# Kernel tuning notes

Hardware: AMD Instinct MI355X
Metric: run time of the kernel (lower is better)

Reference implementation:

```python
import jax, jax.numpy as jnp
import numpy as np

N, F, H, E, C1, C2, NCLS, K = 10000, 64, 128, 640000, 100, 1, 2, 3


def _spmm(rows, cols, vals, x, n):
    # sparse [n,n] @ dense [n,F] via edge list: out[r] += v * x[c]
    return jax.ops.segment_sum(vals[:, None] * x[cols], rows, num_segments=n)


def _cluster(xc, W1, b1, W2, b2):
    # ClusteringLayer: soft assignment s [m,c]; pooled feats [c,F]; corr at input res [m,F]
    h = jax.nn.relu(xc @ W1 + b1)
    s = jax.nn.softmax(h @ W2 + b2, axis=1)
    x_new = s.T @ xc
    corr = s @ x_new
    return x_new, corr, s


def setup_inputs() -> dict:
    key = jax.random.key(0)
    ks = jax.random.split(key, 20)
    sc = 0.05
    return {
        "x": jax.random.normal(ks[0], (N, F), jnp.float32),
        "x_cov": jax.random.normal(ks[1], (N, F), jnp.float32),
        "edge_index": jax.random.randint(ks[2], (2, E), 0, N),
        "adj_vals": jax.random.uniform(ks[3], (E,), jnp.float32),
        "norm_vals": jax.random.uniform(ks[4], (E,), jnp.float32) / 64.0,
        "feature_corr": jax.random.normal(ks[5], (1, F), jnp.float32),
        "bn_gamma": jnp.ones((F,), jnp.float32),
        "bn_beta": jnp.zeros((F,), jnp.float32),
        "pool0_W1": sc * jax.random.normal(ks[6], (F, H), jnp.float32),
        "pool0_b1": jnp.zeros((H,), jnp.float32),
        "pool0_W2": sc * jax.random.normal(ks[7], (H, C1), jnp.float32),
        "pool0_b2": jnp.zeros((C1,), jnp.float32),
        "pool1_W1": sc * jax.random.normal(ks[8], (F, H), jnp.float32),
        "pool1_b1": jnp.zeros((H,), jnp.float32),
        "pool1_W2": sc * jax.random.normal(ks[9], (H, C2), jnp.float32),
        "pool1_b2": jnp.zeros((C2,), jnp.float32),
        "mlp_W1": sc * jax.random.normal(ks[10], (F, H), jnp.float32),
        "mlp_b1": jnp.zeros((H,), jnp.float32),
        "mlp_W2": sc * jax.random.normal(ks[11], (H, H), jnp.float32),
        "mlp_b2": jnp.zeros((H,), jnp.float32),
        "mlp_W3": sc * jax.random.normal(ks[12], (H, NCLS), jnp.float32),
        "mlp_b3": jnp.zeros((NCLS,), jnp.float32),
        "prelu_a": jnp.asarray(0.25, jnp.float32),
    }


def reference(x, x_cov, edge_index, adj_vals, norm_vals, feature_corr,
              bn_gamma, bn_beta,
              pool0_W1, pool0_b1, pool0_W2, pool0_b2,
              pool1_W1, pool1_b1, pool1_W2, pool1_b2,
              mlp_W1, mlp_b1, mlp_W2, mlp_b2, mlp_W3, mlp_b3, prelu_a):
    rows, cols = edge_index[0], edge_index[1]
    n = x.shape[0]
    # BatchNorm1d (batch statistics)
    mu = x.mean(axis=0)
    var = x.var(axis=0)
    x = x0 = (x - mu) / jnp.sqrt(var + 1e-5) * bn_gamma + bn_beta
    # hierarchical pooling (n_pool = 2)
    x_cov1, corr0, s0 = _cluster(x_cov, pool0_W1, pool0_b1, pool0_W2, pool0_b2)   # s0 [N,C1]
    x_cov2, corr1, s1 = _cluster(x_cov1, pool1_W1, pool1_b1, pool1_W2, pool1_b2)  # s1 [C1,1]
    # gains (i=1): 2*sigmoid(masks[1] @ corrs[2] - corrs[1])  -> [C1,F]
    g0 = 2.0 * jax.nn.sigmoid(s1 @ feature_corr - corr1)
    # per-edge diag-mask values: m[e,f] = sum_c s0[r_e,c] * g0[c,f] * s0[c_e,c]
    m = (s0[rows] * s0[cols]) @ g0                      # [E,F]
    # adj is cumulatively multiplied across the feature loop j (adj reused across j)
    adjs = adj_vals[:, None] * jnp.cumprod(m, axis=1)   # [E,F] sparse values on adj pattern
    # Propagation with alpha=0: x = norm_adj @ x, k times (x0 contributes alpha*x0 = 0)
    for _ in range(K):
        x = _spmm(rows, cols, norm_vals, x, n)
    prelu = lambda z: jnp.where(z > 0, z, prelu_a * z)
    h = prelu(x @ mlp_W1 + mlp_b1)
    h = prelu(h @ mlp_W2 + mlp_b2)
    logits = h @ mlp_W3 + mlp_b3
    return jax.nn.log_softmax(logits, axis=1), adjs
```

## Files before the change

### kernel.cpp

```cpp
#include <hip/hip_runtime.h>

#define NN 10000
#define FF 64
#define HH 128
#define EE 640000
#define CC 100

__global__ __launch_bounds__(256) void k_bn_stats(
    const float* __restrict__ x, const float* __restrict__ gamma,
    const float* __restrict__ beta, float* __restrict__ scale, float* __restrict__ shift){
  int f = blockIdx.x, t = threadIdx.x;
  double s = 0.0, s2 = 0.0;
  for (int r = t; r < NN; r += 256){ float v = x[r*FF + f]; s += v; s2 += (double)v * v; }
  #pragma unroll
  for (int o = 32; o > 0; o >>= 1){ s += __shfl_down(s, o); s2 += __shfl_down(s2, o); }
  __shared__ double ls[4], ls2[4];
  if ((t & 63) == 0){ ls[t >> 6] = s; ls2[t >> 6] = s2; }
  __syncthreads();
  if (t == 0){
    double S  = ls[0]+ls[1]+ls[2]+ls[3];
    double S2 = ls2[0]+ls2[1]+ls2[2]+ls2[3];
    double mu = S / NN;
    double var = S2 / NN - mu*mu;
    double sc = (double)gamma[f] / sqrt(var + 1e-5);
    scale[f] = (float)sc;
    shift[f] = (float)((double)beta[f] - mu*sc);
  }
}

__global__ __launch_bounds__(256) void k_hist(const int* __restrict__ rows, int* __restrict__ counts){
  int e = blockIdx.x*256 + threadIdx.x;
  if (e < EE) atomicAdd(&counts[rows[e]], 1);
}

__global__ __launch_bounds__(256) void k_scan(const int* __restrict__ counts,
    int* __restrict__ offs, int* __restrict__ curs){
  __shared__ int part[256];
  int t = threadIdx.x;
  int base = t*40;
  int s = 0;
  for (int i=0;i<40;i++){ int idx=base+i; if (idx<NN) s += counts[idx]; }
  part[t] = s;
  __syncthreads();
  for (int o=1;o<256;o<<=1){
    int v = (t>=o)? part[t-o] : 0;
    __syncthreads();
    part[t] += v;
    __syncthreads();
  }
  int run = (t==0)? 0 : part[t-1];
  for (int i=0;i<40;i++){ int idx=base+i; if (idx<NN){ offs[idx]=run; curs[idx]=run; run += counts[idx]; } }
  if (t==255) offs[NN] = part[255];
}

__global__ __launch_bounds__(256) void k_scatter(const int* __restrict__ rows, const int* __restrict__ cols,
    const float* __restrict__ nvals, int* __restrict__ curs,
    int* __restrict__ cols_s, float* __restrict__ vals_s){
  int e = blockIdx.x*256 + threadIdx.x;
  if (e < EE){
    int r = rows[e];
    int pos = atomicAdd(&curs[r], 1);
    cols_s[pos] = cols[e];
    vals_s[pos] = nvals[e];
  }
}

__global__ __launch_bounds__(256) void k_spmm_bn(
    const int* __restrict__ offs, const int* __restrict__ cols_s, const float* __restrict__ vals_s,
    const float* __restrict__ xin, const float* __restrict__ scale, const float* __restrict__ shift,
    float* __restrict__ xout){
  int lane = threadIdx.x & 63;
  int r = blockIdx.x*4 + (threadIdx.x >> 6);
  float sc = scale[lane], sh = shift[lane];
  int b = offs[r], e = offs[r+1];
  float acc = 0.f;
  for (int j = b; j < e; ++j){
    int c = cols_s[j]; float v = vals_s[j];
    acc += v * (xin[c*FF + lane]*sc + sh);
  }
  xout[r*FF + lane] = acc;
}

__global__ __launch_bounds__(256) void k_spmm(
    const int* __restrict__ offs, const int* __restrict__ cols_s, const float* __restrict__ vals_s,
    const float* __restrict__ xin, float* __restrict__ xout){
  int lane = threadIdx.x & 63;
  int r = blockIdx.x*4 + (threadIdx.x >> 6);
  int b = offs[r], e = offs[r+1];
  float acc = 0.f;
  for (int j = b; j < e; ++j){
    int c = cols_s[j];
    acc += vals_s[j] * xin[c*FF + lane];
  }
  xout[r*FF + lane] = acc;
}

__global__ __launch_bounds__(256) void k_s0(
    const float* __restrict__ xcov,
    const float* __restrict__ W1, const float* __restrict__ b1,
    const float* __restrict__ W2, const float* __restrict__ b2,
    float* __restrict__ s0){
  __shared__ float xs[32][FF];
  __shared__ float hs[32][HH];
  __shared__ float lsm[32][CC];
  __shared__ float chunk[32*HH];
  __shared__ float rsum[32];
  int t = threadIdx.x; int r0 = blockIdx.x*32;
  for (int i=t;i<32*FF;i+=256){ int r=i>>6, f=i&63; int gr=r0+r; xs[r][f] = (gr<NN)? xcov[gr*FF+f] : 0.f; }
  __syncthreads();
  {
    int j = t & 127;
    float acc[16]; float bb = b1[j];
    #pragma unroll
    for (int p=0;p<16;p++) acc[p] = bb;
    for (int kc=0;kc<2;kc++){
      for (int i=t;i<32*HH;i+=256) chunk[i] = W1[(kc*32 + (i>>7))*HH + (i&127)];
      __syncthreads();
      #pragma unroll
      for (int p=0;p<16;p++){
        int r = (t>>7) + 2*p;
        float a = acc[p];
        #pragma unroll
        for (int k=0;k<32;k++) a += xs[r][kc*32+k]*chunk[k*HH + j];
        acc[p] = a;
      }
      __syncthreads();
    }
    #pragma unroll
    for (int p=0;p<16;p++){ int r=(t>>7)+2*p; hs[r][j] = fmaxf(acc[p], 0.f); }
  }
  __syncthreads();
  {
    float acc[13];
    #pragma unroll
    for (int p=0;p<13;p++){ int i=p*256+t; acc[p] = (i<3200)? b2[i % CC] : 0.f; }
    for (int kc=0;kc<4;kc++){
      for (int i=t;i<32*CC;i+=256) chunk[i] = W2[(kc*32 + i/CC)*CC + (i % CC)];
      __syncthreads();
      #pragma unroll
      for (int p=0;p<13;p++){
        int i = p*256+t;
        if (i < 32*CC){
          int r = i/CC, j = i - r*CC;
          float a = acc[p];
          #pragma unroll
          for (int k=0;k<32;k++) a += hs[r][kc*32+k]*chunk[k*CC + j];
          acc[p] = a;
        }
      }
      __syncthreads();
    }
    #pragma unroll
    for (int p=0;p<13;p++){ int i=p*256+t; if (i<32*CC){ int r=i/CC, j=i-r*CC; lsm[r][j]=acc[p]; } }
  }
  __syncthreads();
  if (t < 32){
    float m = -1e30f;
    for (int j=0;j<CC;j++) m = fmaxf(m, lsm[t][j]);
    float s = 0.f;
    for (int j=0;j<CC;j++){ float e = expf(lsm[t][j]-m); lsm[t][j]=e; s += e; }
    rsum[t] = s;
  }
  __syncthreads();
  for (int i=t;i<32*CC;i+=256){ int r=i/CC, j=i-r*CC; int gr=r0+r; if (gr<NN) s0[gr*CC + j] = lsm[r][j]/rsum[r]; }
}

__global__ __launch_bounds__(256) void k_xcov1(
    const float* __restrict__ s0, const float* __restrict__ xcov, float* __restrict__ xc1){
  __shared__ float srow[4][CC];
  __shared__ float xrow[4][FF];
  int t = threadIdx.x;
  int rbase = blockIdx.x * 100;
  int f = t & 63, cb = (t>>6)*25;
  float acc[25];
  #pragma unroll
  for (int i=0;i<25;i++) acc[i]=0.f;
  for (int step=0; step<25; ++step){
    int rr0 = rbase + step*4;
    for (int i=t;i<4*CC;i+=256){ int rr=i/CC; srow[rr][i - rr*CC] = s0[(rr0+rr)*CC + (i - rr*CC)]; }
    for (int i=t;i<4*FF;i+=256){ int rr=i>>6; xrow[rr][i&63] = xcov[(rr0+rr)*FF + (i&63)]; }
    __syncthreads();
    #pragma unroll
    for (int rr=0;rr<4;rr++){
      float xv = xrow[rr][f];
      #pragma unroll
      for (int i=0;i<25;i++) acc[i] += srow[rr][cb+i]*xv;
    }
    __syncthreads();
  }
  #pragma unroll
  for (int i=0;i<25;i++) atomicAdd(&xc1[(cb+i)*FF + f], acc[i]);
}

__global__ void k_gv(const float* __restrict__ xc1, const float* __restrict__ fc, float* __restrict__ gv){
  int f = threadIdx.x;
  float s = 0.f;
  for (int c=0;c<CC;c++) s += xc1[c*FF + f];
  float z = fc[f] - s;
  gv[f] = 2.f / (1.f + expf(-z));
}

__global__ __launch_bounds__(256) void k_adjs(
    const int* __restrict__ rows, const int* __restrict__ cols,
    const float* __restrict__ adjv, const float* __restrict__ s0,
    const float* __restrict__ gv, float* __restrict__ out){
  __shared__ float gvs[64];
  __shared__ int   rs[256], cs[256];
  __shared__ float dotbuf[256];
  __shared__ float buf[16*258];
  int t = threadIdx.x;
  int e0 = blockIdx.x*256;
  rs[t] = rows[e0+t]; cs[t] = cols[e0+t];
  if (t < 64) gvs[t] = gv[t];
  __syncthreads();
  int gid = t>>4, lane = t&15;
  for (int it=0; it<16; ++it){
    int ed = gid*16 + it;
    int r = rs[ed], c = cs[ed];
    const float2* sr = (const float2*)(s0 + (size_t)r*CC);
    const float2* sc2 = (const float2*)(s0 + (size_t)c*CC);
    float p = 0.f;
    #pragma unroll
    for (int k=0;k<4;k++){
      int cc2 = k*16 + lane;
      if (cc2 < 50){
        float2 a = sr[cc2], b = sc2[cc2];
        p += a.x*b.x + a.y*b.y;
      }
    }
    #pragma unroll
    for (int o=1;o<16;o<<=1) p += __shfl_xor(p, o);
    if (lane==0) dotbuf[ed] = p;
  }
  __syncthreads();
  float dot = dotbuf[t];
  float adj = adjv[e0+t];
  float cum = 1.f;
  float4* out4 = (float4*)out;
  size_t obase4 = (size_t)e0*16;
  for (int ch=0; ch<4; ++ch){
    #pragma unroll
    for (int j=0;j<16;j++){
      cum *= dot * gvs[ch*16+j];
      buf[j*258 + t] = adj*cum;
    }
    __syncthreads();
    #pragma unroll
    for (int i=0;i<4;i++){
      int id = i*256 + t;
      int el = id >> 2, f4 = id & 3;
      float4 v;
      v.x = buf[(f4*4+0)*258 + el];
      v.y = buf[(f4*4+1)*258 + el];
      v.z = buf[(f4*4+2)*258 + el];
      v.w = buf[(f4*4+3)*258 + el];
      out4[obase4 + (size_t)el*16 + ch*4 + f4] = v;
    }
    __syncthreads();
  }
}

__global__ __launch_bounds__(256) void k_mlp(
    const float* __restrict__ xin,
    const float* __restrict__ W1, const float* __restrict__ b1,
    const float* __restrict__ W2, const float* __restrict__ b2,
    const float* __restrict__ W3, const float* __restrict__ b3,
    const float* __restrict__ pa, float* __restrict__ out){
  __shared__ float xs[32][FF];
  __shared__ float h1[32][HH];
  __shared__ float h2[32][HH];
  __shared__ float chunk[32*HH];
  __shared__ float lg[32][2];
  int t = threadIdx.x; int r0 = blockIdx.x*32;
  float a0 = pa[0];
  for (int i=t;i<32*FF;i+=256){ int r=i>>6,f=i&63; int gr=r0+r; xs[r][f]=(gr<NN)? xin[gr*FF+f] : 0.f; }
  __syncthreads();
  {
    int j = t & 127;
    float acc[16]; float bb=b1[j];
    #pragma unroll
    for (int p=0;p<16;p++) acc[p]=bb;
    for (int kc=0;kc<2;kc++){
      for (int i=t;i<32*HH;i+=256) chunk[i]=W1[(kc*32+(i>>7))*HH+(i&127)];
      __syncthreads();
      #pragma unroll
      for (int p=0;p<16;p++){ int r=(t>>7)+2*p; float a=acc[p];
        #pragma unroll
        for (int k=0;k<32;k++) a += xs[r][kc*32+k]*chunk[k*HH+j];
        acc[p]=a; }
      __syncthreads();
    }
    #pragma unroll
    for (int p=0;p<16;p++){ int r=(t>>7)+2*p; float v=acc[p]; h1[r][j] = v>0.f? v : a0*v; }
  }
  __syncthreads();
  {
    int j = t & 127;
    float acc[16]; float bb=b2[j];
    #pragma unroll
    for (int p=0;p<16;p++) acc[p]=bb;
    for (int kc=0;kc<4;kc++){
      for (int i=t;i<32*HH;i+=256) chunk[i]=W2[(kc*32+(i>>7))*HH+(i&127)];
      __syncthreads();
      #pragma unroll
      for (int p=0;p<16;p++){ int r=(t>>7)+2*p; float a=acc[p];
        #pragma unroll
        for (int k=0;k<32;k++) a += h1[r][kc*32+k]*chunk[k*HH+j];
        acc[p]=a; }
      __syncthreads();
    }
    #pragma unroll
    for (int p=0;p<16;p++){ int r=(t>>7)+2*p; float v=acc[p]; h2[r][j] = v>0.f? v : a0*v; }
  }
  __syncthreads();
  if (t < 64){
    int cls = t & 1, r = t >> 1;
    float acc = b3[cls];
    #pragma unroll
    for (int k=0;k<HH;k++){
      int kk = (k + r) & 127;
      acc += h2[r][kk]*W3[kk*2+cls];
    }
    lg[r][cls] = acc;
  }
  __syncthreads();
  if (t < 32){
    int gr = r0 + t;
    if (gr < NN){
      float l0=lg[t][0], l1=lg[t][1];
      float m = fmaxf(l0,l1);
      float lse = m + logf(expf(l0-m)+expf(l1-m));
      out[gr*2+0] = l0 - lse;
      out[gr*2+1] = l1 - lse;
    }
  }
}

extern "C" void kernel_launch(void* const* d_in, const int* in_sizes, int n_in,
                              void* d_out, int out_size, void* d_ws, size_t ws_size,
                              hipStream_t stream) {
  (void)in_sizes; (void)n_in; (void)out_size; (void)ws_size;
  const float* x      = (const float*)d_in[0];
  const float* xcov   = (const float*)d_in[1];
  const int*   ei     = (const int*)d_in[2];
  const float* adjv   = (const float*)d_in[3];
  const float* nvals  = (const float*)d_in[4];
  const float* fc     = (const float*)d_in[5];
  const float* gamma  = (const float*)d_in[6];
  const float* beta   = (const float*)d_in[7];
  const float* p0W1   = (const float*)d_in[8];
  const float* p0b1   = (const float*)d_in[9];
  const float* p0W2   = (const float*)d_in[10];
  const float* p0b2   = (const float*)d_in[11];
  const float* mW1    = (const float*)d_in[16];
  const float* mb1    = (const float*)d_in[17];
  const float* mW2    = (const float*)d_in[18];
  const float* mb2    = (const float*)d_in[19];
  const float* mW3    = (const float*)d_in[20];
  const float* mb3    = (const float*)d_in[21];
  const float* pa     = (const float*)d_in[22];
  const int* rows = ei;
  const int* cols = ei + EE;
  float* out = (float*)d_out;

  char* w = (char*)d_ws;
  auto alloc = [&](size_t bytes)->void*{ void* p=(void*)w; w += (bytes + 255) & ~(size_t)255; return p; };
  float* S0    = (float*)alloc(sizeof(float)*(size_t)NN*CC);
  float* XC1   = (float*)alloc(sizeof(float)*CC*FF);
  float* GV    = (float*)alloc(sizeof(float)*FF);
  float* SCALE = (float*)alloc(sizeof(float)*FF);
  float* SHIFT = (float*)alloc(sizeof(float)*FF);
  float* XA    = (float*)alloc(sizeof(float)*(size_t)NN*FF);
  float* XB    = (float*)alloc(sizeof(float)*(size_t)NN*FF);
  int*   COUNTS= (int*)alloc(sizeof(int)*NN);
  int*   OFFS  = (int*)alloc(sizeof(int)*(NN+1));
  int*   CURS  = (int*)alloc(sizeof(int)*NN);
  int*   COLS_S= (int*)alloc(sizeof(int)*EE);
  float* VALS_S= (float*)alloc(sizeof(float)*EE);

  hipMemsetAsync(COUNTS, 0, sizeof(int)*NN, stream);
  hipMemsetAsync(XC1, 0, sizeof(float)*CC*FF, stream);

  k_bn_stats<<<FF, 256, 0, stream>>>(x, gamma, beta, SCALE, SHIFT);
  k_hist<<<EE/256, 256, 0, stream>>>(rows, COUNTS);
  k_scan<<<1, 256, 0, stream>>>(COUNTS, OFFS, CURS);
  k_scatter<<<EE/256, 256, 0, stream>>>(rows, cols, nvals, CURS, COLS_S, VALS_S);

  k_s0<<<(NN+31)/32, 256, 0, stream>>>(xcov, p0W1, p0b1, p0W2, p0b2, S0);
  k_xcov1<<<100, 256, 0, stream>>>(S0, xcov, XC1);
  k_gv<<<1, 64, 0, stream>>>(XC1, fc, GV);
  k_adjs<<<EE/256, 256, 0, stream>>>(rows, cols, adjv, S0, GV, out + 2*NN);

  k_spmm_bn<<<NN/4, 256, 0, stream>>>(OFFS, COLS_S, VALS_S, x, SCALE, SHIFT, XA);
  k_spmm   <<<NN/4, 256, 0, stream>>>(OFFS, COLS_S, VALS_S, XA, XB);
  k_spmm   <<<NN/4, 256, 0, stream>>>(OFFS, COLS_S, VALS_S, XB, XA);

  k_mlp<<<(NN+31)/32, 256, 0, stream>>>(XA, mW1, mb1, mW2, mb2, mW3, mb3, pa, out);
}
```

Measured before the change: 690.3 us.

## Parallelize BN stats, split adjs into dot and stream kernels, unroll SpMM

Batch-norm statistics become a 100-block partial reduction followed by a small finishing kernel, replacing the 64-block per-feature column walk. The scan widens to 1024 threads. The SpMM loops unroll by four with independent accumulators to expose more memory-level parallelism. The per-edge s0 dot products move to their own kernel that uses float4 loads and writes to a new buffer, which the adjs kernel then streams. The s0 and MLP kernels are also reworked: weights are cached in registers, loads are vectorized, and the softmax and logits use shuffle reductions. The extra dot buffer adds an EE-sized write and read, and the new launches add overhead.

```diff
diff --git a/kernel.cpp b/kernel.cpp
--- a/kernel.cpp
+++ b/kernel.cpp
@@ -6,26 +6,35 @@
 #define EE 640000
 #define CC 100
 
-__global__ __launch_bounds__(256) void k_bn_stats(
-    const float* __restrict__ x, const float* __restrict__ gamma,
-    const float* __restrict__ beta, float* __restrict__ scale, float* __restrict__ shift){
-  int f = blockIdx.x, t = threadIdx.x;
+__global__ __launch_bounds__(256) void k_bn_partial(
+    const float* __restrict__ x, double* __restrict__ part){
+  __shared__ double ds[4][64], d2[4][64];
+  int t = threadIdx.x; int f = t & 63, g = t >> 6;
+  size_t base = (size_t)blockIdx.x * 6400;
   double s = 0.0, s2 = 0.0;
-  for (int r = t; r < NN; r += 256){ float v = x[r*FF + f]; s += v; s2 += (double)v * v; }
   #pragma unroll
-  for (int o = 32; o > 0; o >>= 1){ s += __shfl_down(s, o); s2 += __shfl_down(s2, o); }
-  __shared__ double ls[4], ls2[4];
-  if ((t & 63) == 0){ ls[t >> 6] = s; ls2[t >> 6] = s2; }
-  __syncthreads();
-  if (t == 0){
-    double S  = ls[0]+ls[1]+ls[2]+ls[3];
-    double S2 = ls2[0]+ls2[1]+ls2[2]+ls2[3];
-    double mu = S / NN;
-    double var = S2 / NN - mu*mu;
-    double sc = (double)gamma[f] / sqrt(var + 1e-5);
-    scale[f] = (float)sc;
-    shift[f] = (float)((double)beta[f] - mu*sc);
-  }
+  for (int i = 0; i < 25; i++){ float v = x[base + i*256 + t]; s += v; s2 += (double)v * v; }
+  ds[g][f] = s; d2[g][f] = s2;
+  __syncthreads();
+  if (t < 64){
+    double S  = ds[0][t]+ds[1][t]+ds[2][t]+ds[3][t];
+    double S2 = d2[0][t]+d2[1][t]+d2[2][t]+d2[3][t];
+    part[blockIdx.x*128 + t]      = S;
+    part[blockIdx.x*128 + 64 + t] = S2;
+  }
+}
+
+__global__ void k_bn_finish(const double* __restrict__ part,
+    const float* __restrict__ gamma, const float* __restrict__ beta,
+    float* __restrict__ scale, float* __restrict__ shift){
+  int f = threadIdx.x;
+  double S = 0.0, S2 = 0.0;
+  for (int b = 0; b < 100; b++){ S += part[b*128 + f]; S2 += part[b*128 + 64 + f]; }
+  double mu = S / NN;
+  double var = S2 / NN - mu*mu;
+  double sc = (double)gamma[f] / sqrt(var + 1e-5);
+  scale[f] = (float)sc;
+  shift[f] = (float)((double)beta[f] - mu*sc);
 }
 
 __global__ __launch_bounds__(256) void k_hist(const int* __restrict__ rows, int* __restrict__ counts){
@@ -33,24 +42,26 @@
   if (e < EE) atomicAdd(&counts[rows[e]], 1);
 }
 
-__global__ __launch_bounds__(256) void k_scan(const int* __restrict__ counts,
+__global__ __launch_bounds__(1024) void k_scan(const int* __restrict__ counts,
     int* __restrict__ offs, int* __restrict__ curs){
-  __shared__ int part[256];
+  __shared__ int part[1024];
   int t = threadIdx.x;
-  int base = t*40;
+  int base = t*10;
   int s = 0;
-  for (int i=0;i<40;i++){ int idx=base+i; if (idx<NN) s += counts[idx]; }
+  #pragma unroll
+  for (int i=0;i<10;i++){ int idx=base+i; if (idx<NN) s += counts[idx]; }
   part[t] = s;
   __syncthreads();
-  for (int o=1;o<256;o<<=1){
+  for (int o=1;o<1024;o<<=1){
     int v = (t>=o)? part[t-o] : 0;
     __syncthreads();
     part[t] += v;
     __syncthreads();
   }
   int run = (t==0)? 0 : part[t-1];
-  for (int i=0;i<40;i++){ int idx=base+i; if (idx<NN){ offs[idx]=run; curs[idx]=run; run += counts[idx]; } }
-  if (t==255) offs[NN] = part[255];
+  #pragma unroll
+  for (int i=0;i<10;i++){ int idx=base+i; if (idx<NN){ offs[idx]=run; curs[idx]=run; run += counts[idx]; } }
+  if (t==1023) offs[NN] = part[1023];
 }
 
 __global__ __launch_bounds__(256) void k_scatter(const int* __restrict__ rows, const int* __restrict__ cols,
@@ -73,12 +84,18 @@
   int r = blockIdx.x*4 + (threadIdx.x >> 6);
   float sc = scale[lane], sh = shift[lane];
   int b = offs[r], e = offs[r+1];
-  float acc = 0.f;
-  for (int j = b; j < e; ++j){
-    int c = cols_s[j]; float v = vals_s[j];
-    acc += v * (xin[c*FF + lane]*sc + sh);
-  }
-  xout[r*FF + lane] = acc;
+  float a0=0.f,a1=0.f,a2=0.f,a3=0.f;
+  int j = b;
+  for (; j+4<=e; j+=4){
+    int c0=cols_s[j],c1=cols_s[j+1],c2=cols_s[j+2],c3=cols_s[j+3];
+    float v0=vals_s[j],v1=vals_s[j+1],v2=vals_s[j+2],v3=vals_s[j+3];
+    a0 += v0*(xin[(size_t)c0*FF+lane]*sc+sh);
+    a1 += v1*(xin[(size_t)c1*FF+lane]*sc+sh);
+    a2 += v2*(xin[(size_t)c2*FF+lane]*sc+sh);
+    a3 += v3*(xin[(size_t)c3*FF+lane]*sc+sh);
+  }
+  for (; j<e; ++j) a0 += vals_s[j]*(xin[(size_t)cols_s[j]*FF+lane]*sc+sh);
+  xout[(size_t)r*FF + lane] = (a0+a1)+(a2+a3);
 }
 
 __global__ __launch_bounds__(256) void k_spmm(
@@ -87,12 +104,18 @@
   int lane = threadIdx.x & 63;
   int r = blockIdx.x*4 + (threadIdx.x >> 6);
   int b = offs[r], e = offs[r+1];
-  float acc = 0.f;
-  for (int j = b; j < e; ++j){
-    int c = cols_s[j];
-    acc += vals_s[j] * xin[c*FF + lane];
-  }
-  xout[r*FF + lane] = acc;
+  float a0=0.f,a1=0.f,a2=0.f,a3=0.f;
+  int j = b;
+  for (; j+4<=e; j+=4){
+    int c0=cols_s[j],c1=cols_s[j+1],c2=cols_s[j+2],c3=cols_s[j+3];
+    float v0=vals_s[j],v1=vals_s[j+1],v2=vals_s[j+2],v3=vals_s[j+3];
+    a0 += v0*xin[(size_t)c0*FF+lane];
+    a1 += v1*xin[(size_t)c1*FF+lane];
+    a2 += v2*xin[(size_t)c2*FF+lane];
+    a3 += v3*xin[(size_t)c3*FF+lane];
+  }
+  for (; j<e; ++j) a0 += vals_s[j]*xin[(size_t)cols_s[j]*FF+lane];
+  xout[(size_t)r*FF + lane] = (a0+a1)+(a2+a3);
 }
 
 __global__ __launch_bounds__(256) void k_s0(
@@ -101,68 +124,79 @@
     const float* __restrict__ W2, const float* __restrict__ b2,
     float* __restrict__ s0){
   __shared__ float xs[32][FF];
-  __shared__ float hs[32][HH];
-  __shared__ float lsm[32][CC];
+  __shared__ float hs[32][132];
   __shared__ float chunk[32*HH];
-  __shared__ float rsum[32];
   int t = threadIdx.x; int r0 = blockIdx.x*32;
   for (int i=t;i<32*FF;i+=256){ int r=i>>6, f=i&63; int gr=r0+r; xs[r][f] = (gr<NN)? xcov[gr*FF+f] : 0.f; }
   __syncthreads();
   {
-    int j = t & 127;
+    int j = t & 127, rb = t >> 7;
     float acc[16]; float bb = b1[j];
     #pragma unroll
     for (int p=0;p<16;p++) acc[p] = bb;
     for (int kc=0;kc<2;kc++){
       for (int i=t;i<32*HH;i+=256) chunk[i] = W1[(kc*32 + (i>>7))*HH + (i&127)];
       __syncthreads();
+      float cw[32];
+      #pragma unroll
+      for (int k=0;k<32;k++) cw[k] = chunk[k*HH + j];
       #pragma unroll
       for (int p=0;p<16;p++){
-        int r = (t>>7) + 2*p;
+        int r = rb + 2*p;
         float a = acc[p];
         #pragma unroll
-        for (int k=0;k<32;k++) a += xs[r][kc*32+k]*chunk[k*HH + j];
+        for (int k4=0;k4<8;k4++){
+          float4 xq = *(const float4*)&xs[r][kc*32 + k4*4];
+          a += xq.x*cw[k4*4+0]; a += xq.y*cw[k4*4+1];
+          a += xq.z*cw[k4*4+2]; a += xq.w*cw[k4*4+3];
+        }
         acc[p] = a;
       }
       __syncthreads();
     }
     #pragma unroll
-    for (int p=0;p<16;p++){ int r=(t>>7)+2*p; hs[r][j] = fmaxf(acc[p], 0.f); }
+    for (int p=0;p<16;p++){ int r = rb + 2*p; hs[r][j] = fmaxf(acc[p], 0.f); }
   }
   __syncthreads();
   {
+    int r = t >> 3, l = t & 7;
     float acc[13];
     #pragma unroll
-    for (int p=0;p<13;p++){ int i=p*256+t; acc[p] = (i<3200)? b2[i % CC] : 0.f; }
+    for (int q=0;q<13;q++){ int j = l + 8*q; acc[q] = (j < CC)? b2[j] : 0.f; }
     for (int kc=0;kc<4;kc++){
-      for (int i=t;i<32*CC;i+=256) chunk[i] = W2[(kc*32 + i/CC)*CC + (i % CC)];
-      __syncthreads();
-      #pragma unroll
-      for (int p=0;p<13;p++){
-        int i = p*256+t;
-        if (i < 32*CC){
-          int r = i/CC, j = i - r*CC;
-          float a = acc[p];
+      for (int i=t;i<32*104;i+=256){ int kk=i/104, jj=i-kk*104; chunk[i] = (jj<CC)? W2[(kc*32+kk)*CC + jj] : 0.f; }
+      __syncthreads();
+      #pragma unroll
+      for (int k4=0;k4<8;k4++){
+        float4 hq = *(const float4*)&hs[r][kc*32 + k4*4];
+        float hv[4] = {hq.x, hq.y, hq.z, hq.w};
+        #pragma unroll
+        for (int c=0;c<4;c++){
+          float h = hv[c];
+          const float* crow = &chunk[(k4*4+c)*104 + l];
           #pragma unroll
-          for (int k=0;k<32;k++) a += hs[r][kc*32+k]*chunk[k*CC + j];
-          acc[p] = a;
+          for (int q=0;q<13;q++) acc[q] += h * crow[8*q];
         }
       }
       __syncthreads();
     }
-    #pragma unroll
-    for (int p=0;p<13;p++){ int i=p*256+t; if (i<32*CC){ int r=i/CC, j=i-r*CC; lsm[r][j]=acc[p]; } }
-  }
-  __syncthreads();
-  if (t < 32){
-    float m = -1e30f;
-    for (int j=0;j<CC;j++) m = fmaxf(m, lsm[t][j]);
-    float s = 0.f;
-    for (int j=0;j<CC;j++){ float e = expf(lsm[t][j]-m); lsm[t][j]=e; s += e; }
-    rsum[t] = s;
-  }
-  __syncthreads();
-  for (int i=t;i<32*CC;i+=256){ int r=i/CC, j=i-r*CC; int gr=r0+r; if (gr<NN) s0[gr*CC + j] = lsm[r][j]/rsum[r]; }
+    float mx = -1e30f;
+    #pragma unroll
+    for (int q=0;q<13;q++){ if (l + 8*q < CC) mx = fmaxf(mx, acc[q]); }
+    #pragma unroll
+    for (int o=1;o<8;o<<=1) mx = fmaxf(mx, __shfl_xor(mx, o));
+    float sum = 0.f;
+    #pragma unroll
+    for (int q=0;q<13;q++){ if (l + 8*q < CC){ acc[q] = expf(acc[q]-mx); sum += acc[q]; } }
+    #pragma unroll
+    for (int o=1;o<8;o<<=1) sum += __shfl_xor(sum, o);
+    int gr = r0 + r;
+    if (gr < NN){
+      float inv = 1.f/sum;
+      #pragma unroll
+      for (int q=0;q<13;q++){ int j = l + 8*q; if (j < CC) s0[(size_t)gr*CC + j] = acc[q]*inv; }
+    }
+  }
 }
 
 __global__ __launch_bounds__(256) void k_xcov1(
@@ -177,8 +211,8 @@
   for (int i=0;i<25;i++) acc[i]=0.f;
   for (int step=0; step<25; ++step){
     int rr0 = rbase + step*4;
-    for (int i=t;i<4*CC;i+=256){ int rr=i/CC; srow[rr][i - rr*CC] = s0[(rr0+rr)*CC + (i - rr*CC)]; }
-    for (int i=t;i<4*FF;i+=256){ int rr=i>>6; xrow[rr][i&63] = xcov[(rr0+rr)*FF + (i&63)]; }
+    for (int i=t;i<4*CC;i+=256){ int rr=i/CC; srow[rr][i - rr*CC] = s0[(size_t)(rr0+rr)*CC + (i - rr*CC)]; }
+    for (int i=t;i<4*FF;i+=256){ int rr=i>>6; xrow[rr][i&63] = xcov[(size_t)(rr0+rr)*FF + (i&63)]; }
     __syncthreads();
     #pragma unroll
     for (int rr=0;rr<4;rr++){
@@ -200,41 +234,44 @@
   gv[f] = 2.f / (1.f + expf(-z));
 }
 
-__global__ __launch_bounds__(256) void k_adjs(
+__global__ __launch_bounds__(256) void k_dots(
     const int* __restrict__ rows, const int* __restrict__ cols,
-    const float* __restrict__ adjv, const float* __restrict__ s0,
+    const float* __restrict__ s0, float* __restrict__ dotv){
+  __shared__ int rs[256], cs[256];
+  __shared__ float db[256];
+  int t = threadIdx.x; int e0 = blockIdx.x*256;
+  rs[t] = rows[e0+t]; cs[t] = cols[e0+t];
+  __syncthreads();
+  int g = t>>4, lane = t&15;
+  for (int it=0; it<16; ++it){
+    int ed = g*16 + it;
+    const float4* sr = (const float4*)(s0 + (size_t)rs[ed]*CC);
+    const float4* sc = (const float4*)(s0 + (size_t)cs[ed]*CC);
+    float4 a = sr[lane], b = sc[lane];
+    float p = a.x*b.x + a.y*b.y + a.z*b.z + a.w*b.w;
+    if (lane < 9){
+      float4 a2 = sr[16+lane], b2 = sc[16+lane];
+      p += a2.x*b2.x + a2.y*b2.y + a2.z*b2.z + a2.w*b2.w;
+    }
+    #pragma unroll
+    for (int o=1;o<16;o<<=1) p += __shfl_xor(p, o);
+    if (lane==0) db[ed] = p;
+  }
+  __syncthreads();
+  dotv[e0+t] = db[t];
+}
+
+__global__ __launch_bounds__(256) void k_adjs_stream(
+    const float* __restrict__ dotv, const float* __restrict__ adjv,
     const float* __restrict__ gv, float* __restrict__ out){
   __shared__ float gvs[64];
-  __shared__ int   rs[256], cs[256];
-  __shared__ float dotbuf[256];
   __shared__ float buf[16*258];
   int t = threadIdx.x;
   int e0 = blockIdx.x*256;
-  rs[t] = rows[e0+t]; cs[t] = cols[e0+t];
   if (t < 64) gvs[t] = gv[t];
-  __syncthreads();
-  int gid = t>>4, lane = t&15;
-  for (int it=0; it<16; ++it){
-    int ed = gid*16 + it;
-    int r = rs[ed], c = cs[ed];
-    const float2* sr = (const float2*)(s0 + (size_t)r*CC);
-    const float2* sc2 = (const float2*)(s0 + (size_t)c*CC);
-    float p = 0.f;
-    #pragma unroll
-    for (int k=0;k<4;k++){
-      int cc2 = k*16 + lane;
-      if (cc2 < 50){
-        float2 a = sr[cc2], b = sc2[cc2];
-        p += a.x*b.x + a.y*b.y;
-      }
-    }
-    #pragma unroll
-    for (int o=1;o<16;o<<=1) p += __shfl_xor(p, o);
-    if (lane==0) dotbuf[ed] = p;
-  }
-  __syncthreads();
-  float dot = dotbuf[t];
+  float dot = dotv[e0+t];
   float adj = adjv[e0+t];
+  __syncthreads();
   float cum = 1.f;
   float4* out4 = (float4*)out;
   size_t obase4 = (size_t)e0*16;
@@ -268,66 +305,89 @@
     const float* __restrict__ pa, float* __restrict__ out){
   __shared__ float xs[32][FF];
   __shared__ float h1[32][HH];
-  __shared__ float h2[32][HH];
+  __shared__ float h2[32][132];
   __shared__ float chunk[32*HH];
-  __shared__ float lg[32][2];
+  __shared__ float w3s[HH*2];
   int t = threadIdx.x; int r0 = blockIdx.x*32;
   float a0 = pa[0];
   for (int i=t;i<32*FF;i+=256){ int r=i>>6,f=i&63; int gr=r0+r; xs[r][f]=(gr<NN)? xin[gr*FF+f] : 0.f; }
+  for (int i=t;i<HH*2;i+=256) w3s[i] = W3[i];
   __syncthreads();
   {
-    int j = t & 127;
+    int j = t & 127, rb = t >> 7;
     float acc[16]; float bb=b1[j];
     #pragma unroll
     for (int p=0;p<16;p++) acc[p]=bb;
     for (int kc=0;kc<2;kc++){
       for (int i=t;i<32*HH;i+=256) chunk[i]=W1[(kc*32+(i>>7))*HH+(i&127)];
       __syncthreads();
-      #pragma unroll
-      for (int p=0;p<16;p++){ int r=(t>>7)+2*p; float a=acc[p];
+      float cw[32];
+      #pragma unroll
+      for (int k=0;k<32;k++) cw[k] = chunk[k*HH + j];
+      #pragma unroll
+      for (int p=0;p<16;p++){
+        int r = rb + 2*p;
+        float a = acc[p];
         #pragma unroll
-        for (int k=0;k<32;k++) a += xs[r][kc*32+k]*chunk[k*HH+j];
-        acc[p]=a; }
-      __syncthreads();
-    }
-    #pragma unroll
-    for (int p=0;p<16;p++){ int r=(t>>7)+2*p; float v=acc[p]; h1[r][j] = v>0.f? v : a0*v; }
+        for (int k4=0;k4<8;k4++){
+          float4 xq = *(const float4*)&xs[r][kc*32 + k4*4];
+          a += xq.x*cw[k4*4+0]; a += xq.y*cw[k4*4+1];
+          a += xq.z*cw[k4*4+2]; a += xq.w*cw[k4*4+3];
+        }
+        acc[p] = a;
+      }
+      __syncthreads();
+    }
+    #pragma unroll
+    for (int p=0;p<16;p++){ int r=rb+2*p; float v=acc[p]; h1[r][j] = v>0.f? v : a0*v; }
   }
   __syncthreads();
   {
-    int j = t & 127;
+    int j = t & 127, rb = t >> 7;
     float acc[16]; float bb=b2[j];
     #pragma unroll
     for (int p=0;p<16;p++) acc[p]=bb;
     for (int kc=0;kc<4;kc++){
       for (int i=t;i<32*HH;i+=256) chunk[i]=W2[(kc*32+(i>>7))*HH+(i&127)];
       __syncthreads();
-      #pragma unroll
-      for (int p=0;p<16;p++){ int r=(t>>7)+2*p; float a=acc[p];
+      float cw[32];
+      #pragma unroll
+      for (int k=0;k<32;k++) cw[k] = chunk[k*HH + j];
+      #pragma unroll
+      for (int p=0;p<16;p++){
+        int r = rb + 2*p;
+        float a = acc[p];
         #pragma unroll
-        for (int k=0;k<32;k++) a += h1[r][kc*32+k]*chunk[k*HH+j];
-        acc[p]=a; }
-      __syncthreads();
-    }
-    #pragma unroll
-    for (int p=0;p<16;p++){ int r=(t>>7)+2*p; float v=acc[p]; h2[r][j] = v>0.f? v : a0*v; }
-  }
-  __syncthreads();
-  if (t < 64){
-    int cls = t & 1, r = t >> 1;
-    float acc = b3[cls];
-    #pragma unroll
-    for (int k=0;k<HH;k++){
-      int kk = (k + r) & 127;
-      acc += h2[r][kk]*W3[kk*2+cls];
-    }
-    lg[r][cls] = acc;
-  }
-  __syncthreads();
-  if (t < 32){
-    int gr = r0 + t;
-    if (gr < NN){
-      float l0=lg[t][0], l1=lg[t][1];
+        for (int k4=0;k4<8;k4++){
+          float4 xq = *(const float4*)&h1[r][kc*32 + k4*4];
+          a += xq.x*cw[k4*4+0]; a += xq.y*cw[k4*4+1];
+          a += xq.z*cw[k4*4+2]; a += xq.w*cw[k4*4+3];
+        }
+        acc[p] = a;
+      }
+      __syncthreads();
+    }
+    #pragma unroll
+    for (int p=0;p<16;p++){ int r=rb+2*p; float v=acc[p]; h2[r][t&127] = v>0.f? v : a0*v; }
+  }
+  __syncthreads();
+  {
+    int r = t >> 3, l = t & 7;
+    float aA = 0.f, aB = 0.f;
+    #pragma unroll
+    for (int n=0;n<4;n++){
+      float4 hq = *(const float4*)&h2[r][l*16 + n*4];
+      int kb = l*16 + n*4;
+      aA += hq.x*w3s[(kb+0)*2+0]; aB += hq.x*w3s[(kb+0)*2+1];
+      aA += hq.y*w3s[(kb+1)*2+0]; aB += hq.y*w3s[(kb+1)*2+1];
+      aA += hq.z*w3s[(kb+2)*2+0]; aB += hq.z*w3s[(kb+2)*2+1];
+      aA += hq.w*w3s[(kb+3)*2+0]; aB += hq.w*w3s[(kb+3)*2+1];
+    }
+    #pragma unroll
+    for (int o=1;o<8;o<<=1){ aA += __shfl_xor(aA,o); aB += __shfl_xor(aB,o); }
+    int gr = r0 + r;
+    if (l==0 && gr < NN){
+      float l0 = aA + b3[0], l1 = aB + b3[1];
       float m = fmaxf(l0,l1);
       float lse = m + logf(expf(l0-m)+expf(l1-m));
       out[gr*2+0] = l0 - lse;
@@ -365,31 +425,35 @@
 
   char* w = (char*)d_ws;
   auto alloc = [&](size_t bytes)->void*{ void* p=(void*)w; w += (bytes + 255) & ~(size_t)255; return p; };
-  float* S0    = (float*)alloc(sizeof(float)*(size_t)NN*CC);
-  float* XC1   = (float*)alloc(sizeof(float)*CC*FF);
-  float* GV    = (float*)alloc(sizeof(float)*FF);
-  float* SCALE = (float*)alloc(sizeof(float)*FF);
-  float* SHIFT = (float*)alloc(sizeof(float)*FF);
-  float* XA    = (float*)alloc(sizeof(float)*(size_t)NN*FF);
-  float* XB    = (float*)alloc(sizeof(float)*(size_t)NN*FF);
-  int*   COUNTS= (int*)alloc(sizeof(int)*NN);
-  int*   OFFS  = (int*)alloc(sizeof(int)*(NN+1));
-  int*   CURS  = (int*)alloc(sizeof(int)*NN);
-  int*   COLS_S= (int*)alloc(sizeof(int)*EE);
-  float* VALS_S= (float*)alloc(sizeof(float)*EE);
+  float*  S0    = (float*)alloc(sizeof(float)*(size_t)NN*CC);
+  float*  XC1   = (float*)alloc(sizeof(float)*CC*FF);
+  float*  GV    = (float*)alloc(sizeof(float)*FF);
+  float*  SCALE = (float*)alloc(sizeof(float)*FF);
+  float*  SHIFT = (float*)alloc(sizeof(float)*FF);
+  float*  XA    = (float*)alloc(sizeof(float)*(size_t)NN*FF);
+  float*  XB    = (float*)alloc(sizeof(float)*(size_t)NN*FF);
+  int*    COUNTS= (int*)alloc(sizeof(int)*NN);
+  int*    OFFS  = (int*)alloc(sizeof(int)*(NN+1));
+  int*    CURS  = (int*)alloc(sizeof(int)*NN);
+  int*    COLS_S= (int*)alloc(sizeof(int)*EE);
+  float*  VALS_S= (float*)alloc(sizeof(float)*EE);
+  float*  DOTV  = (float*)alloc(sizeof(float)*EE);
+  double* BNP   = (double*)alloc(sizeof(double)*100*128);
 
   hipMemsetAsync(COUNTS, 0, sizeof(int)*NN, stream);
   hipMemsetAsync(XC1, 0, sizeof(float)*CC*FF, stream);
 
-  k_bn_stats<<<FF, 256, 0, stream>>>(x, gamma, beta, SCALE, SHIFT);
+  k_bn_partial<<<100, 256, 0, stream>>>(x, BNP);
+  k_bn_finish<<<1, 64, 0, stream>>>(BNP, gamma, beta, SCALE, SHIFT);
   k_hist<<<EE/256, 256, 0, stream>>>(rows, COUNTS);
-  k_scan<<<1, 256, 0, stream>>>(COUNTS, OFFS, CURS);
+  k_scan<<<1, 1024, 0, stream>>>(COUNTS, OFFS, CURS);
   k_scatter<<<EE/256, 256, 0, stream>>>(rows, cols, nvals, CURS, COLS_S, VALS_S);
 
   k_s0<<<(NN+31)/32, 256, 0, stream>>>(xcov, p0W1, p0b1, p0W2, p0b2, S0);
+  k_dots<<<EE/256, 256, 0, stream>>>(rows, cols, S0, DOTV);
   k_xcov1<<<100, 256, 0, stream>>>(S0, xcov, XC1);
   k_gv<<<1, 64, 0, stream>>>(XC1, fc, GV);
-  k_adjs<<<EE/256, 256, 0, stream>>>(rows, cols, adjv, S0, GV, out + 2*NN);
+  k_adjs_stream<<<EE/256, 256, 0, stream>>>(DOTV, adjv, GV, out + 2*NN);
 
   k_spmm_bn<<<NN/4, 256, 0, stream>>>(OFFS, COLS_S, VALS_S, x, SCALE, SHIFT, XA);
   k_spmm   <<<NN/4, 256, 0, stream>>>(OFFS, COLS_S, VALS_S, XA, XB);
```

New measurement: 565.7 us. 18.1% less time.
